# Kernel tuning notes

Hardware: AMD Instinct MI355X
Metric: run time of the kernel (lower is better)

The kernel has to match this reference:

```python
import jax, jax.numpy as jnp
import numpy as np

EPS_LN = 1e-5
EPS_OPM = 1e-3

# dims
S, N, CM, CZ, CH, H, DH = 512, 256, 64, 128, 32, 8, 32
FF = 4 * CM


def _ln(x, w, b):
    mu = jnp.mean(x, axis=-1, keepdims=True)
    var = jnp.mean((x - mu) ** 2, axis=-1, keepdims=True)
    return (x - mu) / jnp.sqrt(var + EPS_LN) * w + b


def setup_inputs() -> dict:
    key = jax.random.key(0)
    ks = jax.random.split(key, 16)
    def w(k, shape):
        return jax.random.normal(k, shape, dtype=jnp.float32) / np.sqrt(shape[0])
    inp = {
        'm': jax.random.normal(ks[0], (S, N, CM), dtype=jnp.float32),
        'z': jax.random.normal(ks[1], (N, N, CZ), dtype=jnp.float32),
        'msa_mask': jnp.ones((S, N), dtype=jnp.float32),
        # OuterProductMean params
        'opm_ln_w': jnp.ones((CM,), jnp.float32), 'opm_ln_b': jnp.zeros((CM,), jnp.float32),
        'opm_w1': w(ks[2], (CM, CH)), 'opm_w2': w(ks[3], (CM, CH)),
        'opm_wout': w(ks[4], (CH * CH, CZ)), 'opm_bout': jnp.zeros((CZ,), jnp.float32),
        # MSAPairWeightedAveraging params
        'pwa_lnm_w': jnp.ones((CM,), jnp.float32), 'pwa_lnm_b': jnp.zeros((CM,), jnp.float32),
        'pwa_lnz_w': jnp.ones((CZ,), jnp.float32), 'pwa_lnz_b': jnp.zeros((CZ,), jnp.float32),
        'pwa_wv': w(ks[5], (CM, H * DH)), 'pwa_wz': w(ks[6], (CZ, H)),
        'pwa_wg': w(ks[7], (CM, H * DH)), 'pwa_wo': w(ks[8], (H * DH, CM)),
        # Transition (SwiGLU, factor 4) params
        'tr_ln_w': jnp.ones((CM,), jnp.float32), 'tr_ln_b': jnp.zeros((CM,), jnp.float32),
        'tr_wa': w(ks[9], (CM, FF)), 'tr_wb': w(ks[10], (CM, FF)), 'tr_wo': w(ks[11], (FF, CM)),
    }
    return inp


def reference(m, z, msa_mask,
              opm_ln_w, opm_ln_b, opm_w1, opm_w2, opm_wout, opm_bout,
              pwa_lnm_w, pwa_lnm_b, pwa_lnz_w, pwa_lnz_b, pwa_wv, pwa_wz, pwa_wg, pwa_wo,
              tr_ln_w, tr_ln_b, tr_wa, tr_wb, tr_wo):
    s, n, cm = m.shape
    h = pwa_wz.shape[1]
    dh = pwa_wv.shape[1] // h
    ch = opm_w1.shape[1]
    # ---- OuterProductMean: z += OPM(m) ----
    mn = _ln(m, opm_ln_w, opm_ln_b)
    mk = msa_mask[..., None]                           # (S, N, 1)
    norm = jnp.einsum('sac,sdc->adc', mk, mk)          # (N, N, 1)
    a = (mn @ opm_w1) * mk                             # (S, N, CH)
    b = (mn @ opm_w2) * mk
    outer = jnp.einsum('sic,sje->ijce', a, b).reshape(n, n, ch * ch)
    z = z + (outer @ opm_wout + opm_bout) / (norm + EPS_OPM)
    # ---- MSAPairWeightedAveraging (residual) ----
    w_att = jax.nn.softmax(_ln(z, pwa_lnz_w, pwa_lnz_b) @ pwa_wz, axis=-2)  # (N, N, H), softmax over j
    mn2 = _ln(m, pwa_lnm_w, pwa_lnm_b)
    v = (mn2 @ pwa_wv).reshape(s, n, h, dh)
    g = jax.nn.sigmoid(mn2 @ pwa_wg).reshape(s, n, h, dh)
    o = jnp.einsum('ijh,sjhd->sihd', w_att, v)
    m = m + (g * o).reshape(s, n, h * dh) @ pwa_wo
    # ---- Transition (SwiGLU, factor 4, residual) ----
    x = _ln(m, tr_ln_w, tr_ln_b)
    m = m + (jax.nn.silu(x @ tr_wa) * (x @ tr_wb)) @ tr_wo
    return (m, z)
```

## Files before the change

### kernel.cpp

```cpp
#include <hip/hip_runtime.h>
#include <hip/hip_bf16.h>

#define S 512
#define N 256
#define CM 64
#define CZ 128
#define CH 32
#define H 8
#define DH 32
#define FF 256
#define HDH 256

typedef __attribute__((ext_vector_type(8))) short bf16x8;
typedef __attribute__((ext_vector_type(4))) float f32x4;

__device__ __forceinline__ float waveReduceSum(float v) {
    #pragma unroll
    for (int off = 32; off > 0; off >>= 1) v += __shfl_xor(v, off);
    return v;
}
__device__ __forceinline__ float waveReduceMax(float v) {
    #pragma unroll
    for (int off = 32; off > 0; off >>= 1) v = fmaxf(v, __shfl_xor(v, off));
    return v;
}
__device__ __forceinline__ unsigned short f2bf(float x) {
    __hip_bfloat16 h = __float2bfloat16(x);
    return *reinterpret_cast<unsigned short*>(&h);
}
__device__ __forceinline__ float bfbits2f(short u) {
    unsigned int x = ((unsigned int)(unsigned short)u) << 16;
    return __uint_as_float(x);
}
__device__ __forceinline__ void gload_lds16(const void* g, void* l) {
    __builtin_amdgcn_global_load_lds(
        (const __attribute__((address_space(1))) unsigned int*)g,
        (__attribute__((address_space(3))) unsigned int*)l, 16, 0, 0);
}

__global__ __launch_bounds__(256) void k0_prep(
    const float* __restrict__ wout, const float* __restrict__ wv,
    const float* __restrict__ wg, const float* __restrict__ wa,
    const float* __restrict__ wb, const float* __restrict__ wo,
    const float* __restrict__ wo2,
    __hip_bfloat16* __restrict__ wout_t, __hip_bfloat16* __restrict__ wv_t,
    __hip_bfloat16* __restrict__ wg_t, __hip_bfloat16* __restrict__ wab_t,
    __hip_bfloat16* __restrict__ wo_t, __hip_bfloat16* __restrict__ wo2_t) {
    int idx = blockIdx.x * 256 + threadIdx.x;
    if (idx < 131072) {
        int f = idx >> 10, k = idx & 1023;
        wout_t[idx] = __float2bfloat16(wout[k * 128 + f]);
    } else if (idx < 147456) {
        int t = idx - 131072; int n = t >> 6, k = t & 63;
        wv_t[t] = __float2bfloat16(wv[k * 256 + n]);
    } else if (idx < 163840) {
        int t = idx - 147456; int n = t >> 6, k = t & 63;
        wg_t[t] = __float2bfloat16(wg[k * 256 + n]);
    } else if (idx < 196608) {
        int t = idx - 163840; int n = t >> 6, k = t & 63;
        wab_t[t] = __float2bfloat16(n < 256 ? wa[k * 256 + n] : wb[k * 256 + (n - 256)]);
    } else if (idx < 212992) {
        int t = idx - 196608; int n = t >> 8, k = t & 255;
        wo_t[t] = __float2bfloat16(wo[k * 64 + n]);
    } else if (idx < 229376) {
        int t = idx - 212992; int n = t >> 8, k = t & 255;
        wo2_t[t] = __float2bfloat16(wo2[k * 64 + n]);
    }
}

__global__ __launch_bounds__(256) void k1_ab(
    const float* __restrict__ m, const float* __restrict__ mask,
    const float* __restrict__ lnw, const float* __restrict__ lnb,
    const float* __restrict__ w1, const float* __restrict__ w2,
    __hip_bfloat16* __restrict__ a_t, __hip_bfloat16* __restrict__ b_t) {
    __shared__ float mn[64][64];
    __shared__ float mk[64];
    int tid = threadIdx.x, w = tid >> 6, lane = tid & 63;
    int i = blockIdx.x >> 3, s0 = (blockIdx.x & 7) * 64;
    float lw = lnw[lane], lb = lnb[lane];
    for (int rr = 0; rr < 16; ++rr) {
        int sl = w * 16 + rr;
        float x = m[((size_t)(s0 + sl) * 256 + i) * 64 + lane];
        float mu = waveReduceSum(x) * (1.0f / 64.0f);
        float d = x - mu;
        float var = waveReduceSum(d * d) * (1.0f / 64.0f);
        mn[sl][lane] = d * rsqrtf(var + 1e-5f) * lw + lb;
        if (lane == 0) mk[sl] = mask[(s0 + sl) * 256 + i];
    }
    __syncthreads();
    int e = lane & 31;
    const float* W = (lane < 32) ? w1 : w2;
    __hip_bfloat16* dst = (lane < 32) ? a_t : b_t;
    float acc[16];
    #pragma unroll
    for (int ss = 0; ss < 16; ++ss) acc[ss] = 0.f;
    for (int c = 0; c < 64; ++c) {
        float wc = W[c * 32 + e];
        #pragma unroll
        for (int ss = 0; ss < 16; ++ss)
            acc[ss] += mn[w * 16 + ss][c] * wc;
    }
    __hip_bfloat16 outv[16];
    #pragma unroll
    for (int ss = 0; ss < 16; ++ss)
        outv[ss] = __float2bfloat16(acc[ss] * mk[w * 16 + ss]);
    __hip_bfloat16* p = dst + (size_t)(i * 32 + e) * 512 + s0 + w * 16;
    *(bf16x8*)p = *(bf16x8*)&outv[0];
    *(bf16x8*)(p + 8) = *(bf16x8*)&outv[8];
}

__global__ __launch_bounds__(256) void k1b_norm(
    const float* __restrict__ mask, float* __restrict__ normb) {
    __shared__ float mcol[512];
    int i = blockIdx.x, t = threadIdx.x;
    mcol[t] = mask[t * 256 + i];
    mcol[t + 256] = mask[(t + 256) * 256 + i];
    __syncthreads();
    float acc = 0.f;
    for (int s = 0; s < 512; ++s) acc += mcol[s] * mask[s * 256 + t];
    normb[i * 256 + t] = acc;
}

__global__ __launch_bounds__(256) void k2_opm(
    const __hip_bfloat16* __restrict__ a_t, const __hip_bfloat16* __restrict__ b_t,
    const __hip_bfloat16* __restrict__ wout_t, const float* __restrict__ bout,
    const float* __restrict__ normb, const float* __restrict__ zin,
    float* __restrict__ zout) {
    __shared__ __align__(16) char smem[32768];
    char* As = smem;
    char* Bs = smem + 8192;
    int tid = threadIdx.x;
    int wid = tid >> 6, lane = tid & 63;
    int g = lane >> 4, lc = lane & 15;
    int bm = blockIdx.x >> 6, bn = blockIdx.x & 63;
    int m0 = bm * 128, n0 = bn * 128;
    int wm = wid >> 1, wn = wid & 1;

    f32x4 acc[4][4];
    #pragma unroll
    for (int fm = 0; fm < 4; ++fm)
        #pragma unroll
        for (int fn = 0; fn < 4; ++fn)
            acc[fm][fn] = (f32x4){0.f, 0.f, 0.f, 0.f};

    for (int k0 = 0; k0 < 512; k0 += 32) {
        __syncthreads();
        #pragma unroll
        for (int h = 0; h < 2; ++h) {
            int c = h * 256 + wid * 64 + lane;
            int r = c >> 2, gs = c & 3;
            int gk = gs ^ ((r >> 1) & 3);
            const __hip_bfloat16* ga = a_t + (size_t)(m0 + r) * 512 + k0 + gk * 8;
            const __hip_bfloat16* gb = b_t + (size_t)(n0 + r) * 512 + k0 + gk * 8;
            gload_lds16(ga, As + h * 4096 + wid * 1024);
            gload_lds16(gb, Bs + h * 4096 + wid * 1024);
        }
        __syncthreads();
        bf16x8 af[4], bfr[4];
        #pragma unroll
        for (int fm = 0; fm < 4; ++fm) {
            int row = wm * 64 + fm * 16 + lc;
            int sw = (g * 16) ^ (((row >> 1) & 3) << 4);
            af[fm] = *(bf16x8*)(As + row * 64 + sw);
        }
        #pragma unroll
        for (int fn = 0; fn < 4; ++fn) {
            int row = wn * 64 + fn * 16 + lc;
            int sw = (g * 16) ^ (((row >> 1) & 3) << 4);
            bfr[fn] = *(bf16x8*)(Bs + row * 64 + sw);
        }
        #pragma unroll
        for (int fm = 0; fm < 4; ++fm)
            #pragma unroll
            for (int fn = 0; fn < 4; ++fn)
                acc[fm][fn] = __builtin_amdgcn_mfma_f32_16x16x32_bf16(
                    af[fm], bfr[fn], acc[fm][fn], 0, 0, 0);
    }
    __syncthreads();
    #pragma unroll
    for (int fm = 0; fm < 4; ++fm) {
        int i_loc = wm * 2 + (fm >> 1);
        #pragma unroll
        for (int fn = 0; fn < 4; ++fn) {
            int j_loc = wn * 2 + (fn >> 1);
            int pair = i_loc * 4 + j_loc;
            int xorp = (pair & 7) << 4;
            #pragma unroll
            for (int r = 0; r < 4; ++r) {
                int mm31 = (fm & 1) * 16 + g * 4 + r;
                int nn31 = (fn & 1) * 16 + lc;
                int off = mm31 * 64 + nn31 * 2;
                int offs = off ^ xorp ^ (((off >> 8) & 3) << 4);
                *(unsigned short*)(smem + pair * 2048 + offs) = f2bf(acc[fm][fn][r]);
            }
        }
    }
    __syncthreads();
    f32x4 acc2[2];
    acc2[0] = (f32x4){0.f, 0.f, 0.f, 0.f};
    acc2[1] = (f32x4){0.f, 0.f, 0.f, 0.f};
    int f0 = wid * 32;
    int pr = lc;
    int xorp2 = (pr & 7) << 4;
    for (int k2 = 0; k2 < 1024; k2 += 32) {
        int offA = k2 * 2 + g * 16;
        int offAs = offA ^ xorp2 ^ (((offA >> 8) & 3) << 4);
        bf16x8 af2 = *(bf16x8*)(smem + pr * 2048 + offAs);
        #pragma unroll
        for (int fn2 = 0; fn2 < 2; ++fn2) {
            int f = f0 + fn2 * 16 + lc;
            bf16x8 bw = *(const bf16x8*)(wout_t + (size_t)f * 1024 + k2 + g * 8);
            acc2[fn2] = __builtin_amdgcn_mfma_f32_16x16x32_bf16(af2, bw, acc2[fn2], 0, 0, 0);
        }
    }
    #pragma unroll
    for (int fn2 = 0; fn2 < 2; ++fn2) {
        #pragma unroll
        for (int r = 0; r < 4; ++r) {
            int pair = g * 4 + r;
            int i = bm * 4 + (pair >> 2), j = bn * 4 + (pair & 3);
            int ij = i * 256 + j;
            int f = f0 + fn2 * 16 + lc;
            float d = acc2[fn2][r];
            zout[(size_t)ij * 128 + f] = zin[(size_t)ij * 128 + f] +
                (d + bout[f]) / (normb[ij] + 1e-3f);
        }
    }
}

__global__ __launch_bounds__(256) void k3_logits(
    const float* __restrict__ zout, const float* __restrict__ lnzw,
    const float* __restrict__ lnzb, const float* __restrict__ wz,
    float* __restrict__ wl) {
    __shared__ float znL[4][128];
    int tid = threadIdx.x, w = tid >> 6, lane = tid & 63;
    int pair = blockIdx.x * 4 + w;
    float z0 = zout[pair * 128 + lane];
    float z1 = zout[pair * 128 + 64 + lane];
    float mu = waveReduceSum(z0 + z1) * (1.0f / 128.0f);
    float d0 = z0 - mu, d1 = z1 - mu;
    float var = waveReduceSum(d0 * d0 + d1 * d1) * (1.0f / 128.0f);
    float rstd = rsqrtf(var + 1e-5f);
    znL[w][lane] = d0 * rstd * lnzw[lane] + lnzb[lane];
    znL[w][lane + 64] = d1 * rstd * lnzw[lane + 64] + lnzb[lane + 64];
    __syncthreads();
    int h = lane >> 3, chunk = lane & 7;
    float p = 0.f;
    #pragma unroll
    for (int cc = 0; cc < 16; ++cc) {
        int c = chunk * 16 + cc;
        p += znL[w][c] * wz[c * 8 + h];
    }
    p += __shfl_xor(p, 1); p += __shfl_xor(p, 2); p += __shfl_xor(p, 4);
    if (chunk == 0) {
        int i = pair >> 8, j = pair & 255;
        wl[(i * 8 + h) * 256 + j] = p;
    }
}

__global__ __launch_bounds__(256) void k4_softmax(
    const float* __restrict__ wl, __hip_bfloat16* __restrict__ wlb) {
    __shared__ float red[8];
    int row = blockIdx.x, t = threadIdx.x;
    int w = t >> 6, lane = t & 63;
    float v = wl[row * 256 + t];
    float mx = waveReduceMax(v);
    if (lane == 0) red[w] = mx;
    __syncthreads();
    mx = fmaxf(fmaxf(red[0], red[1]), fmaxf(red[2], red[3]));
    float ex = expf(v - mx);
    float sm = waveReduceSum(ex);
    if (lane == 0) red[4 + w] = sm;
    __syncthreads();
    float tot = red[4] + red[5] + red[6] + red[7];
    int i = row >> 3, h = row & 7;
    wlb[((h << 8) | i) * 256 + t] = __float2bfloat16(ex / tot);
}

__global__ __launch_bounds__(256) void k5vg(
    const float* __restrict__ m, const float* __restrict__ lnw,
    const float* __restrict__ lnb, const __hip_bfloat16* __restrict__ Bt,
    __hip_bfloat16* __restrict__ out, int mode) {
    __shared__ __align__(16) char As[64 * 128];
    int tid = threadIdx.x, wid = tid >> 6, lane = tid & 63;
    int g = lane >> 4, lc = lane & 15;
    int r0 = blockIdx.x * 64;
    float lw = lnw[lane], lb = lnb[lane];
    for (int rr = 0; rr < 16; ++rr) {
        int lr = wid * 16 + rr;
        float x = m[(size_t)(r0 + lr) * 64 + lane];
        float mu = waveReduceSum(x) * (1.0f / 64.0f);
        float d = x - mu;
        float var = waveReduceSum(d * d) * (1.0f / 64.0f);
        float xn = d * rsqrtf(var + 1e-5f) * lw + lb;
        int byt = lr * 128 + ((lane * 2) ^ ((lr & 7) << 4));
        *(unsigned short*)(As + byt) = f2bf(xn);
    }
    __syncthreads();
    int lr = wid * 16 + lc;
    int swz = (lr & 7) << 4;
    bf16x8 af0 = *(bf16x8*)(As + lr * 128 + ((g * 16) ^ swz));
    bf16x8 af1 = *(bf16x8*)(As + lr * 128 + ((64 + g * 16) ^ swz));
    f32x4 acc[16];
    #pragma unroll
    for (int fn = 0; fn < 16; ++fn) acc[fn] = (f32x4){0.f, 0.f, 0.f, 0.f};
    #pragma unroll
    for (int fn = 0; fn < 16; ++fn) {
        bf16x8 b0 = *(const bf16x8*)&Bt[(fn * 16 + lc) * 64 + g * 8];
        bf16x8 b1 = *(const bf16x8*)&Bt[(fn * 16 + lc) * 64 + 32 + g * 8];
        acc[fn] = __builtin_amdgcn_mfma_f32_16x16x32_bf16(af0, b0, acc[fn], 0, 0, 0);
        acc[fn] = __builtin_amdgcn_mfma_f32_16x16x32_bf16(af1, b1, acc[fn], 0, 0, 0);
    }
    if (mode == 0) {
        #pragma unroll
        for (int fn = 0; fn < 16; ++fn) {
            #pragma unroll
            for (int r = 0; r < 4; ++r) {
                int row = r0 + wid * 16 + g * 4 + r;
                int col = fn * 16 + lc;
                int h = col >> 5, d = col & 31;
                int s = row >> 8, j = row & 255;
                out[(size_t)((h << 14) + (s << 5) + d) * 256 + j] = __float2bfloat16(acc[fn][r]);
            }
        }
    } else {
        #pragma unroll
        for (int fn = 0; fn < 16; ++fn) {
            #pragma unroll
            for (int r = 0; r < 4; ++r) {
                int row = r0 + wid * 16 + g * 4 + r;
                int col = fn * 16 + lc;
                float sg = 1.0f / (1.0f + expf(-acc[fn][r]));
                out[(size_t)row * 256 + col] = __float2bfloat16(sg);
            }
        }
    }
}

__global__ __launch_bounds__(256) void k6a(
    const __hip_bfloat16* __restrict__ vb, const __hip_bfloat16* __restrict__ wlb,
    __hip_bfloat16* __restrict__ obuf) {
    __shared__ __align__(16) char smem[16384];
    char* As = smem;
    char* Bs = smem + 8192;
    int tid = threadIdx.x;
    int wid = tid >> 6, lane = tid & 63;
    int g = lane >> 4, lc = lane & 15;
    int idx = blockIdx.x;
    int h = idx >> 8, rem = idx & 255;
    int bm = rem >> 1, bn = rem & 1;
    int m0 = bm * 128, n0 = bn * 128;
    int wm = wid >> 1, wn = wid & 1;
    const __hip_bfloat16* vb_h = vb + (size_t)h * 16384 * 256;
    const __hip_bfloat16* wlb_h = wlb + (size_t)h * 256 * 256;

    f32x4 acc[4][4];
    #pragma unroll
    for (int fm = 0; fm < 4; ++fm)
        #pragma unroll
        for (int fn = 0; fn < 4; ++fn)
            acc[fm][fn] = (f32x4){0.f, 0.f, 0.f, 0.f};

    for (int k0 = 0; k0 < 256; k0 += 32) {
        __syncthreads();
        #pragma unroll
        for (int hh = 0; hh < 2; ++hh) {
            int c = hh * 256 + wid * 64 + lane;
            int r = c >> 2, gs = c & 3;
            int gk = gs ^ ((r >> 1) & 3);
            const __hip_bfloat16* ga = vb_h + (size_t)(m0 + r) * 256 + k0 + gk * 8;
            const __hip_bfloat16* gb = wlb_h + (size_t)(n0 + r) * 256 + k0 + gk * 8;
            gload_lds16(ga, As + hh * 4096 + wid * 1024);
            gload_lds16(gb, Bs + hh * 4096 + wid * 1024);
        }
        __syncthreads();
        bf16x8 af[4], bfr[4];
        #pragma unroll
        for (int fm = 0; fm < 4; ++fm) {
            int row = wm * 64 + fm * 16 + lc;
            int sw = (g * 16) ^ (((row >> 1) & 3) << 4);
            af[fm] = *(bf16x8*)(As + row * 64 + sw);
        }
        #pragma unroll
        for (int fn = 0; fn < 4; ++fn) {
            int row = wn * 64 + fn * 16 + lc;
            int sw = (g * 16) ^ (((row >> 1) & 3) << 4);
            bfr[fn] = *(bf16x8*)(Bs + row * 64 + sw);
        }
        #pragma unroll
        for (int fm = 0; fm < 4; ++fm)
            #pragma unroll
            for (int fn = 0; fn < 4; ++fn)
                acc[fm][fn] = __builtin_amdgcn_mfma_f32_16x16x32_bf16(
                    af[fm], bfr[fn], acc[fm][fn], 0, 0, 0);
    }
    #pragma unroll
    for (int fm = 0; fm < 4; ++fm) {
        #pragma unroll
        for (int fn = 0; fn < 4; ++fn) {
            #pragma unroll
            for (int r = 0; r < 4; ++r) {
                int mm = m0 + wm * 64 + fm * 16 + g * 4 + r;
                int nn = n0 + wn * 64 + fn * 16 + lc;
                int s = mm >> 5, d = mm & 31;
                obuf[(size_t)(s * 256 + nn) * 256 + h * 32 + d] = __float2bfloat16(acc[fm][fn][r]);
            }
        }
    }
}

__global__ __launch_bounds__(256) void k6b(
    const __hip_bfloat16* __restrict__ obuf, const __hip_bfloat16* __restrict__ gsig,
    const __hip_bfloat16* __restrict__ wo_t, const float* __restrict__ m,
    float* __restrict__ mout) {
    int tid = threadIdx.x, wid = tid >> 6, lane = tid & 63;
    int g = lane >> 4, lc = lane & 15;
    int r0 = blockIdx.x * 128;
    f32x4 acc[2][4];
    #pragma unroll
    for (int fm = 0; fm < 2; ++fm)
        #pragma unroll
        for (int fn = 0; fn < 4; ++fn)
            acc[fm][fn] = (f32x4){0.f, 0.f, 0.f, 0.f};
    for (int ks = 0; ks < 8; ++ks) {
        bf16x8 af[2];
        #pragma unroll
        for (int fm = 0; fm < 2; ++fm) {
            int arow = r0 + wid * 32 + fm * 16 + lc;
            bf16x8 ao = *(const bf16x8*)&obuf[(size_t)arow * 256 + ks * 32 + g * 8];
            bf16x8 ag = *(const bf16x8*)&gsig[(size_t)arow * 256 + ks * 32 + g * 8];
            #pragma unroll
            for (int t = 0; t < 8; ++t)
                af[fm][t] = (short)f2bf(bfbits2f(ao[t]) * bfbits2f(ag[t]));
        }
        #pragma unroll
        for (int fn = 0; fn < 4; ++fn) {
            bf16x8 bf_ = *(const bf16x8*)&wo_t[(fn * 16 + lc) * 256 + ks * 32 + g * 8];
            acc[0][fn] = __builtin_amdgcn_mfma_f32_16x16x32_bf16(af[0], bf_, acc[0][fn], 0, 0, 0);
            acc[1][fn] = __builtin_amdgcn_mfma_f32_16x16x32_bf16(af[1], bf_, acc[1][fn], 0, 0, 0);
        }
    }
    #pragma unroll
    for (int fm = 0; fm < 2; ++fm)
        #pragma unroll
        for (int fn = 0; fn < 4; ++fn)
            #pragma unroll
            for (int r = 0; r < 4; ++r) {
                int row = r0 + wid * 32 + fm * 16 + g * 4 + r;
                int col = fn * 16 + lc;
                mout[(size_t)row * 64 + col] = m[(size_t)row * 64 + col] + acc[fm][fn][r];
            }
}

__global__ __launch_bounds__(256) void k7b(
    const float* __restrict__ mbuf, const float* __restrict__ lnw,
    const float* __restrict__ lnb, const __hip_bfloat16* __restrict__ wab_t,
    __hip_bfloat16* __restrict__ hbuf) {
    __shared__ __align__(16) char As[64 * 128];
    int tid = threadIdx.x, wid = tid >> 6, lane = tid & 63;
    int g = lane >> 4, lc = lane & 15;
    int r0 = blockIdx.x * 64;
    float lw = lnw[lane], lb = lnb[lane];
    for (int rr = 0; rr < 16; ++rr) {
        int lr = wid * 16 + rr;
        float x = mbuf[(size_t)(r0 + lr) * 64 + lane];
        float mu = waveReduceSum(x) * (1.0f / 64.0f);
        float d = x - mu;
        float var = waveReduceSum(d * d) * (1.0f / 64.0f);
        float xn = d * rsqrtf(var + 1e-5f) * lw + lb;
        int byt = lr * 128 + ((lane * 2) ^ ((lr & 7) << 4));
        *(unsigned short*)(As + byt) = f2bf(xn);
    }
    __syncthreads();
    int lr = wid * 16 + lc;
    int swz = (lr & 7) << 4;
    bf16x8 af0 = *(bf16x8*)(As + lr * 128 + ((g * 16) ^ swz));
    bf16x8 af1 = *(bf16x8*)(As + lr * 128 + ((64 + g * 16) ^ swz));
    f32x4 acc[32];
    #pragma unroll
    for (int fn = 0; fn < 32; ++fn) acc[fn] = (f32x4){0.f, 0.f, 0.f, 0.f};
    #pragma unroll
    for (int fn = 0; fn < 32; ++fn) {
        bf16x8 b0 = *(const bf16x8*)&wab_t[(fn * 16 + lc) * 64 + g * 8];
        bf16x8 b1 = *(const bf16x8*)&wab_t[(fn * 16 + lc) * 64 + 32 + g * 8];
        acc[fn] = __builtin_amdgcn_mfma_f32_16x16x32_bf16(af0, b0, acc[fn], 0, 0, 0);
        acc[fn] = __builtin_amdgcn_mfma_f32_16x16x32_bf16(af1, b1, acc[fn], 0, 0, 0);
    }
    #pragma unroll
    for (int fn = 0; fn < 16; ++fn) {
        #pragma unroll
        for (int r = 0; r < 4; ++r) {
            int row = r0 + wid * 16 + g * 4 + r;
            int f = fn * 16 + lc;
            float aa = acc[fn][r];
            float bb = acc[fn + 16][r];
            float sil = aa / (1.0f + expf(-aa));
            hbuf[(size_t)row * 256 + f] = __float2bfloat16(sil * bb);
        }
    }
}

__global__ __launch_bounds__(256) void k7c(
    const __hip_bfloat16* __restrict__ hbuf, const __hip_bfloat16* __restrict__ wo2_t,
    float* __restrict__ mout) {
    int tid = threadIdx.x, wid = tid >> 6, lane = tid & 63;
    int g = lane >> 4, lc = lane & 15;
    int r0 = blockIdx.x * 128;
    f32x4 acc[2][4];
    #pragma unroll
    for (int fm = 0; fm < 2; ++fm)
        #pragma unroll
        for (int fn = 0; fn < 4; ++fn)
            acc[fm][fn] = (f32x4){0.f, 0.f, 0.f, 0.f};
    for (int ks = 0; ks < 8; ++ks) {
        bf16x8 af[2];
        #pragma unroll
        for (int fm = 0; fm < 2; ++fm) {
            int arow = r0 + wid * 32 + fm * 16 + lc;
            af[fm] = *(const bf16x8*)&hbuf[(size_t)arow * 256 + ks * 32 + g * 8];
        }
        #pragma unroll
        for (int fn = 0; fn < 4; ++fn) {
            bf16x8 bf_ = *(const bf16x8*)&wo2_t[(fn * 16 + lc) * 256 + ks * 32 + g * 8];
            acc[0][fn] = __builtin_amdgcn_mfma_f32_16x16x32_bf16(af[0], bf_, acc[0][fn], 0, 0, 0);
            acc[1][fn] = __builtin_amdgcn_mfma_f32_16x16x32_bf16(af[1], bf_, acc[1][fn], 0, 0, 0);
        }
    }
    #pragma unroll
    for (int fm = 0; fm < 2; ++fm)
        #pragma unroll
        for (int fn = 0; fn < 4; ++fn)
            #pragma unroll
            for (int r = 0; r < 4; ++r) {
                int row = r0 + wid * 32 + fm * 16 + g * 4 + r;
                int col = fn * 16 + lc;
                mout[(size_t)row * 64 + col] += acc[fm][fn][r];
            }
}

extern "C" void kernel_launch(void* const* d_in, const int* in_sizes, int n_in,
                              void* d_out, int out_size, void* d_ws, size_t ws_size,
                              hipStream_t stream) {
    const float* m        = (const float*)d_in[0];
    const float* z        = (const float*)d_in[1];
    const float* mask     = (const float*)d_in[2];
    const float* opm_ln_w = (const float*)d_in[3];
    const float* opm_ln_b = (const float*)d_in[4];
    const float* opm_w1   = (const float*)d_in[5];
    const float* opm_w2   = (const float*)d_in[6];
    const float* opm_wout = (const float*)d_in[7];
    const float* opm_bout = (const float*)d_in[8];
    const float* pwa_lnm_w = (const float*)d_in[9];
    const float* pwa_lnm_b = (const float*)d_in[10];
    const float* pwa_lnz_w = (const float*)d_in[11];
    const float* pwa_lnz_b = (const float*)d_in[12];
    const float* pwa_wv   = (const float*)d_in[13];
    const float* pwa_wz   = (const float*)d_in[14];
    const float* pwa_wg   = (const float*)d_in[15];
    const float* pwa_wo   = (const float*)d_in[16];
    const float* tr_ln_w  = (const float*)d_in[17];
    const float* tr_ln_b  = (const float*)d_in[18];
    const float* tr_wa    = (const float*)d_in[19];
    const float* tr_wb    = (const float*)d_in[20];
    const float* tr_wo    = (const float*)d_in[21];

    float* m_out = (float*)d_out;
    float* z_out = m_out + (size_t)S * N * CM;

    char* w = (char*)d_ws;
    __hip_bfloat16* wout_t = (__hip_bfloat16*)w;
    __hip_bfloat16* wv_t   = (__hip_bfloat16*)(w + 262144);
    __hip_bfloat16* wg_t   = (__hip_bfloat16*)(w + 294912);
    __hip_bfloat16* wab_t  = (__hip_bfloat16*)(w + 327680);
    __hip_bfloat16* wo_t   = (__hip_bfloat16*)(w + 393216);
    __hip_bfloat16* wo2_t  = (__hip_bfloat16*)(w + 425984);
    float* normb           = (float*)(w + 458752);
    float* wl              = (float*)(w + 720896);
    __hip_bfloat16* wlb    = (__hip_bfloat16*)(w + 2818048);
    char* bufA             = w + 3866624;
    char* bufB             = w + 70975488;

    __hip_bfloat16* a_t  = (__hip_bfloat16*)bufA;
    __hip_bfloat16* b_t  = a_t + 4194304;
    __hip_bfloat16* vb   = (__hip_bfloat16*)bufA;
    __hip_bfloat16* gsig = (__hip_bfloat16*)bufA;
    __hip_bfloat16* obuf = (__hip_bfloat16*)bufB;
    __hip_bfloat16* hbuf = (__hip_bfloat16*)bufB;

    k0_prep<<<896, 256, 0, stream>>>(opm_wout, pwa_wv, pwa_wg, tr_wa, tr_wb, pwa_wo, tr_wo,
                                     wout_t, wv_t, wg_t, wab_t, wo_t, wo2_t);
    k1_ab<<<2048, 256, 0, stream>>>(m, mask, opm_ln_w, opm_ln_b, opm_w1, opm_w2, a_t, b_t);
    k1b_norm<<<N, 256, 0, stream>>>(mask, normb);
    k2_opm<<<4096, 256, 0, stream>>>(a_t, b_t, wout_t, opm_bout, normb, z, z_out);
    k3_logits<<<N * N / 4, 256, 0, stream>>>(z_out, pwa_lnz_w, pwa_lnz_b, pwa_wz, wl);
    k4_softmax<<<N * H, 256, 0, stream>>>(wl, wlb);
    k5vg<<<2048, 256, 0, stream>>>(m, pwa_lnm_w, pwa_lnm_b, wv_t, vb, 0);
    k6a<<<2048, 256, 0, stream>>>(vb, wlb, obuf);
    k5vg<<<2048, 256, 0, stream>>>(m, pwa_lnm_w, pwa_lnm_b, wg_t, gsig, 1);
    k6b<<<1024, 256, 0, stream>>>(obuf, gsig, wo_t, m, m_out);
    k7b<<<2048, 256, 0, stream>>>(m_out, tr_ln_w, tr_ln_b, wab_t, hbuf);
    k7c<<<1024, 256, 0, stream>>>(hbuf, wo2_t, m_out);
}
```

Baseline: 827.0 us.

## Double-buffer LDS in OPM and attention GEMMs; fuse gate, output projection and transition kernel

Adds two-stage LDS double buffering to the k2_opm and k6a GEMM main loops, so the next K tile's global-to-LDS loads are issued before computing on the current tile and one barrier per iteration is removed. It also fuses the sigmoid gate computation, gated output projection plus residual, transition LayerNorm, SwiGLU and output projection into a single per-64-row kernel. The gate and hidden activations stay in shared memory instead of round-tripping through global bf16 buffers, and four launches collapse to one. In exchange, shared memory per block grows (about 58KB in the fused kernel, 32KB in the GEMMs), which may lower occupancy.

```diff
diff --git a/kernel.cpp b/kernel.cpp
--- a/kernel.cpp
+++ b/kernel.cpp
@@ -127,8 +127,6 @@
     const float* __restrict__ normb, const float* __restrict__ zin,
     float* __restrict__ zout) {
     __shared__ __align__(16) char smem[32768];
-    char* As = smem;
-    char* Bs = smem + 8192;
     int tid = threadIdx.x;
     int wid = tid >> 6, lane = tid & 63;
     int g = lane >> 4, lc = lane & 15;
@@ -136,6 +134,7 @@
     int m0 = bm * 128, n0 = bn * 128;
     int wm = wid >> 1, wn = wid & 1;
 
+    int c_ = wid * 64 + lane;
     f32x4 acc[4][4];
     #pragma unroll
     for (int fm = 0; fm < 4; ++fm)
@@ -143,19 +142,26 @@
         for (int fn = 0; fn < 4; ++fn)
             acc[fm][fn] = (f32x4){0.f, 0.f, 0.f, 0.f};
 
-    for (int k0 = 0; k0 < 512; k0 += 32) {
-        __syncthreads();
+    auto stage = [&](int sel, int k0) {
         #pragma unroll
         for (int h = 0; h < 2; ++h) {
-            int c = h * 256 + wid * 64 + lane;
+            int c = h * 256 + c_;
             int r = c >> 2, gs = c & 3;
             int gk = gs ^ ((r >> 1) & 3);
             const __hip_bfloat16* ga = a_t + (size_t)(m0 + r) * 512 + k0 + gk * 8;
             const __hip_bfloat16* gb = b_t + (size_t)(n0 + r) * 512 + k0 + gk * 8;
-            gload_lds16(ga, As + h * 4096 + wid * 1024);
-            gload_lds16(gb, Bs + h * 4096 + wid * 1024);
-        }
-        __syncthreads();
+            gload_lds16(ga, smem + sel * 16384 + h * 4096 + wid * 1024);
+            gload_lds16(gb, smem + sel * 16384 + 8192 + h * 4096 + wid * 1024);
+        }
+    };
+
+    stage(0, 0);
+    __syncthreads();
+    int cur = 0;
+    for (int t = 0; t < 16; ++t) {
+        if (t < 15) stage(cur ^ 1, (t + 1) * 32);
+        char* As = smem + cur * 16384;
+        char* Bs = As + 8192;
         bf16x8 af[4], bfr[4];
         #pragma unroll
         for (int fm = 0; fm < 4; ++fm) {
@@ -175,8 +181,9 @@
             for (int fn = 0; fn < 4; ++fn)
                 acc[fm][fn] = __builtin_amdgcn_mfma_f32_16x16x32_bf16(
                     af[fm], bfr[fn], acc[fm][fn], 0, 0, 0);
-    }
-    __syncthreads();
+        __syncthreads();
+        cur ^= 1;
+    }
     #pragma unroll
     for (int fm = 0; fm < 4; ++fm) {
         int i_loc = wm * 2 + (fm >> 1);
@@ -277,10 +284,10 @@
     wlb[((h << 8) | i) * 256 + t] = __float2bfloat16(ex / tot);
 }
 
-__global__ __launch_bounds__(256) void k5vg(
+__global__ __launch_bounds__(256) void k5v(
     const float* __restrict__ m, const float* __restrict__ lnw,
     const float* __restrict__ lnb, const __hip_bfloat16* __restrict__ Bt,
-    __hip_bfloat16* __restrict__ out, int mode) {
+    __hip_bfloat16* __restrict__ out) {
     __shared__ __align__(16) char As[64 * 128];
     int tid = threadIdx.x, wid = tid >> 6, lane = tid & 63;
     int g = lane >> 4, lc = lane & 15;
@@ -311,28 +318,15 @@
         acc[fn] = __builtin_amdgcn_mfma_f32_16x16x32_bf16(af0, b0, acc[fn], 0, 0, 0);
         acc[fn] = __builtin_amdgcn_mfma_f32_16x16x32_bf16(af1, b1, acc[fn], 0, 0, 0);
     }
-    if (mode == 0) {
-        #pragma unroll
-        for (int fn = 0; fn < 16; ++fn) {
-            #pragma unroll
-            for (int r = 0; r < 4; ++r) {
-                int row = r0 + wid * 16 + g * 4 + r;
-                int col = fn * 16 + lc;
-                int h = col >> 5, d = col & 31;
-                int s = row >> 8, j = row & 255;
-                out[(size_t)((h << 14) + (s << 5) + d) * 256 + j] = __float2bfloat16(acc[fn][r]);
-            }
-        }
-    } else {
-        #pragma unroll
-        for (int fn = 0; fn < 16; ++fn) {
-            #pragma unroll
-            for (int r = 0; r < 4; ++r) {
-                int row = r0 + wid * 16 + g * 4 + r;
-                int col = fn * 16 + lc;
-                float sg = 1.0f / (1.0f + expf(-acc[fn][r]));
-                out[(size_t)row * 256 + col] = __float2bfloat16(sg);
-            }
+    #pragma unroll
+    for (int fn = 0; fn < 16; ++fn) {
+        #pragma unroll
+        for (int r = 0; r < 4; ++r) {
+            int row = r0 + wid * 16 + g * 4 + r;
+            int col = fn * 16 + lc;
+            int h = col >> 5, d = col & 31;
+            int s = row >> 8, j = row & 255;
+            out[(size_t)((h << 14) + (s << 5) + d) * 256 + j] = __float2bfloat16(acc[fn][r]);
         }
     }
 }
@@ -340,9 +334,7 @@
 __global__ __launch_bounds__(256) void k6a(
     const __hip_bfloat16* __restrict__ vb, const __hip_bfloat16* __restrict__ wlb,
     __hip_bfloat16* __restrict__ obuf) {
-    __shared__ __align__(16) char smem[16384];
-    char* As = smem;
-    char* Bs = smem + 8192;
+    __shared__ __align__(16) char smem[32768];
     int tid = threadIdx.x;
     int wid = tid >> 6, lane = tid & 63;
     int g = lane >> 4, lc = lane & 15;
@@ -353,6 +345,7 @@
     int wm = wid >> 1, wn = wid & 1;
     const __hip_bfloat16* vb_h = vb + (size_t)h * 16384 * 256;
     const __hip_bfloat16* wlb_h = wlb + (size_t)h * 256 * 256;
+    int c_ = wid * 64 + lane;
 
     f32x4 acc[4][4];
     #pragma unroll
@@ -361,19 +354,26 @@
         for (int fn = 0; fn < 4; ++fn)
             acc[fm][fn] = (f32x4){0.f, 0.f, 0.f, 0.f};
 
-    for (int k0 = 0; k0 < 256; k0 += 32) {
-        __syncthreads();
+    auto stage = [&](int sel, int k0) {
         #pragma unroll
         for (int hh = 0; hh < 2; ++hh) {
-            int c = hh * 256 + wid * 64 + lane;
+            int c = hh * 256 + c_;
             int r = c >> 2, gs = c & 3;
             int gk = gs ^ ((r >> 1) & 3);
             const __hip_bfloat16* ga = vb_h + (size_t)(m0 + r) * 256 + k0 + gk * 8;
             const __hip_bfloat16* gb = wlb_h + (size_t)(n0 + r) * 256 + k0 + gk * 8;
-            gload_lds16(ga, As + hh * 4096 + wid * 1024);
-            gload_lds16(gb, Bs + hh * 4096 + wid * 1024);
-        }
-        __syncthreads();
+            gload_lds16(ga, smem + sel * 16384 + hh * 4096 + wid * 1024);
+            gload_lds16(gb, smem + sel * 16384 + 8192 + hh * 4096 + wid * 1024);
+        }
+    };
+
+    stage(0, 0);
+    __syncthreads();
+    int cur = 0;
+    for (int t = 0; t < 8; ++t) {
+        if (t < 7) stage(cur ^ 1, (t + 1) * 32);
+        char* As = smem + cur * 16384;
+        char* Bs = As + 8192;
         bf16x8 af[4], bfr[4];
         #pragma unroll
         for (int fm = 0; fm < 4; ++fm) {
@@ -393,6 +393,8 @@
             for (int fn = 0; fn < 4; ++fn)
                 acc[fm][fn] = __builtin_amdgcn_mfma_f32_16x16x32_bf16(
                     af[fm], bfr[fn], acc[fm][fn], 0, 0, 0);
+        __syncthreads();
+        cur ^= 1;
     }
     #pragma unroll
     for (int fm = 0; fm < 4; ++fm) {
@@ -409,133 +411,140 @@
     }
 }
 
-__global__ __launch_bounds__(256) void k6b(
-    const __hip_bfloat16* __restrict__ obuf, const __hip_bfloat16* __restrict__ gsig,
-    const __hip_bfloat16* __restrict__ wo_t, const float* __restrict__ m,
+__global__ __launch_bounds__(256) void k67(
+    const float* __restrict__ m,
+    const float* __restrict__ lnmw, const float* __restrict__ lnmb,
+    const __hip_bfloat16* __restrict__ wg_t, const __hip_bfloat16* __restrict__ wo_t,
+    const __hip_bfloat16* __restrict__ obuf,
+    const float* __restrict__ trlnw, const float* __restrict__ trlnb,
+    const __hip_bfloat16* __restrict__ wab_t, const __hip_bfloat16* __restrict__ wo2_t,
     float* __restrict__ mout) {
-    int tid = threadIdx.x, wid = tid >> 6, lane = tid & 63;
-    int g = lane >> 4, lc = lane & 15;
-    int r0 = blockIdx.x * 128;
-    f32x4 acc[2][4];
-    #pragma unroll
-    for (int fm = 0; fm < 2; ++fm)
-        #pragma unroll
-        for (int fn = 0; fn < 4; ++fn)
-            acc[fm][fn] = (f32x4){0.f, 0.f, 0.f, 0.f};
-    for (int ks = 0; ks < 8; ++ks) {
-        bf16x8 af[2];
-        #pragma unroll
-        for (int fm = 0; fm < 2; ++fm) {
-            int arow = r0 + wid * 32 + fm * 16 + lc;
-            bf16x8 ao = *(const bf16x8*)&obuf[(size_t)arow * 256 + ks * 32 + g * 8];
-            bf16x8 ag = *(const bf16x8*)&gsig[(size_t)arow * 256 + ks * 32 + g * 8];
-            #pragma unroll
-            for (int t = 0; t < 8; ++t)
-                af[fm][t] = (short)f2bf(bfbits2f(ao[t]) * bfbits2f(ag[t]));
-        }
-        #pragma unroll
-        for (int fn = 0; fn < 4; ++fn) {
-            bf16x8 bf_ = *(const bf16x8*)&wo_t[(fn * 16 + lc) * 256 + ks * 32 + g * 8];
-            acc[0][fn] = __builtin_amdgcn_mfma_f32_16x16x32_bf16(af[0], bf_, acc[0][fn], 0, 0, 0);
-            acc[1][fn] = __builtin_amdgcn_mfma_f32_16x16x32_bf16(af[1], bf_, acc[1][fn], 0, 0, 0);
-        }
-    }
-    #pragma unroll
-    for (int fm = 0; fm < 2; ++fm)
-        #pragma unroll
-        for (int fn = 0; fn < 4; ++fn)
-            #pragma unroll
-            for (int r = 0; r < 4; ++r) {
-                int row = r0 + wid * 32 + fm * 16 + g * 4 + r;
-                int col = fn * 16 + lc;
-                mout[(size_t)row * 64 + col] = m[(size_t)row * 64 + col] + acc[fm][fn][r];
-            }
-}
-
-__global__ __launch_bounds__(256) void k7b(
-    const float* __restrict__ mbuf, const float* __restrict__ lnw,
-    const float* __restrict__ lnb, const __hip_bfloat16* __restrict__ wab_t,
-    __hip_bfloat16* __restrict__ hbuf) {
-    __shared__ __align__(16) char As[64 * 128];
+    __shared__ __align__(16) char xnS[8192];
+    __shared__ __align__(16) char ghS[32768];
+    __shared__ float mnS[64][68];
     int tid = threadIdx.x, wid = tid >> 6, lane = tid & 63;
     int g = lane >> 4, lc = lane & 15;
     int r0 = blockIdx.x * 64;
-    float lw = lnw[lane], lb = lnb[lane];
-    for (int rr = 0; rr < 16; ++rr) {
-        int lr = wid * 16 + rr;
-        float x = mbuf[(size_t)(r0 + lr) * 64 + lane];
-        float mu = waveReduceSum(x) * (1.0f / 64.0f);
-        float d = x - mu;
-        float var = waveReduceSum(d * d) * (1.0f / 64.0f);
-        float xn = d * rsqrtf(var + 1e-5f) * lw + lb;
-        int byt = lr * 128 + ((lane * 2) ^ ((lr & 7) << 4));
-        *(unsigned short*)(As + byt) = f2bf(xn);
-    }
-    __syncthreads();
     int lr = wid * 16 + lc;
     int swz = (lr & 7) << 4;
-    bf16x8 af0 = *(bf16x8*)(As + lr * 128 + ((g * 16) ^ swz));
-    bf16x8 af1 = *(bf16x8*)(As + lr * 128 + ((64 + g * 16) ^ swz));
-    f32x4 acc[32];
-    #pragma unroll
-    for (int fn = 0; fn < 32; ++fn) acc[fn] = (f32x4){0.f, 0.f, 0.f, 0.f};
-    #pragma unroll
-    for (int fn = 0; fn < 32; ++fn) {
-        bf16x8 b0 = *(const bf16x8*)&wab_t[(fn * 16 + lc) * 64 + g * 8];
-        bf16x8 b1 = *(const bf16x8*)&wab_t[(fn * 16 + lc) * 64 + 32 + g * 8];
-        acc[fn] = __builtin_amdgcn_mfma_f32_16x16x32_bf16(af0, b0, acc[fn], 0, 0, 0);
-        acc[fn] = __builtin_amdgcn_mfma_f32_16x16x32_bf16(af1, b1, acc[fn], 0, 0, 0);
-    }
-    #pragma unroll
-    for (int fn = 0; fn < 16; ++fn) {
-        #pragma unroll
-        for (int r = 0; r < 4; ++r) {
-            int row = r0 + wid * 16 + g * 4 + r;
-            int f = fn * 16 + lc;
-            float aa = acc[fn][r];
-            float bb = acc[fn + 16][r];
-            float sil = aa / (1.0f + expf(-aa));
-            hbuf[(size_t)row * 256 + f] = __float2bfloat16(sil * bb);
-        }
-    }
-}
-
-__global__ __launch_bounds__(256) void k7c(
-    const __hip_bfloat16* __restrict__ hbuf, const __hip_bfloat16* __restrict__ wo2_t,
-    float* __restrict__ mout) {
-    int tid = threadIdx.x, wid = tid >> 6, lane = tid & 63;
-    int g = lane >> 4, lc = lane & 15;
-    int r0 = blockIdx.x * 128;
-    f32x4 acc[2][4];
-    #pragma unroll
-    for (int fm = 0; fm < 2; ++fm)
+
+    {
+        float lw = lnmw[lane], lb = lnmb[lane];
+        for (int rr = 0; rr < 16; ++rr) {
+            int r2 = wid * 16 + rr;
+            float x = m[(size_t)(r0 + r2) * 64 + lane];
+            float mu = waveReduceSum(x) * (1.0f / 64.0f);
+            float d = x - mu;
+            float var = waveReduceSum(d * d) * (1.0f / 64.0f);
+            float xn = d * rsqrtf(var + 1e-5f) * lw + lb;
+            *(unsigned short*)(xnS + r2 * 128 + ((lane * 2) ^ ((r2 & 7) << 4))) = f2bf(xn);
+        }
+    }
+    __syncthreads();
+    {
+        bf16x8 af0 = *(bf16x8*)(xnS + lr * 128 + ((g * 16) ^ swz));
+        bf16x8 af1 = *(bf16x8*)(xnS + lr * 128 + ((64 + g * 16) ^ swz));
+        #pragma unroll
+        for (int fn = 0; fn < 16; ++fn) {
+            f32x4 a_ = (f32x4){0.f, 0.f, 0.f, 0.f};
+            bf16x8 b0 = *(const bf16x8*)&wg_t[(fn * 16 + lc) * 64 + g * 8];
+            bf16x8 b1 = *(const bf16x8*)&wg_t[(fn * 16 + lc) * 64 + 32 + g * 8];
+            a_ = __builtin_amdgcn_mfma_f32_16x16x32_bf16(af0, b0, a_, 0, 0, 0);
+            a_ = __builtin_amdgcn_mfma_f32_16x16x32_bf16(af1, b1, a_, 0, 0, 0);
+            #pragma unroll
+            for (int r = 0; r < 4; ++r) {
+                int row = wid * 16 + g * 4 + r, col = fn * 16 + lc;
+                float sg = 1.0f / (1.0f + expf(-a_[r]));
+                *(unsigned short*)(ghS + row * 512 + ((col * 2) ^ ((row & 7) << 4))) = f2bf(sg);
+            }
+        }
+    }
+    __syncthreads();
+    {
+        f32x4 acc[4];
+        #pragma unroll
+        for (int fn = 0; fn < 4; ++fn) acc[fn] = (f32x4){0.f, 0.f, 0.f, 0.f};
+        for (int ks = 0; ks < 8; ++ks) {
+            bf16x8 ao = *(const bf16x8*)&obuf[(size_t)(r0 + lr) * 256 + ks * 32 + g * 8];
+            bf16x8 ag = *(bf16x8*)(ghS + lr * 512 + ((ks * 64 + g * 16) ^ swz));
+            bf16x8 af;
+            #pragma unroll
+            for (int t = 0; t < 8; ++t)
+                af[t] = (short)f2bf(bfbits2f(ao[t]) * bfbits2f(ag[t]));
+            #pragma unroll
+            for (int fn = 0; fn < 4; ++fn) {
+                bf16x8 bf_ = *(const bf16x8*)&wo_t[(fn * 16 + lc) * 256 + ks * 32 + g * 8];
+                acc[fn] = __builtin_amdgcn_mfma_f32_16x16x32_bf16(af, bf_, acc[fn], 0, 0, 0);
+            }
+        }
         #pragma unroll
         for (int fn = 0; fn < 4; ++fn)
-            acc[fm][fn] = (f32x4){0.f, 0.f, 0.f, 0.f};
-    for (int ks = 0; ks < 8; ++ks) {
-        bf16x8 af[2];
-        #pragma unroll
-        for (int fm = 0; fm < 2; ++fm) {
-            int arow = r0 + wid * 32 + fm * 16 + lc;
-            af[fm] = *(const bf16x8*)&hbuf[(size_t)arow * 256 + ks * 32 + g * 8];
-        }
-        #pragma unroll
-        for (int fn = 0; fn < 4; ++fn) {
-            bf16x8 bf_ = *(const bf16x8*)&wo2_t[(fn * 16 + lc) * 256 + ks * 32 + g * 8];
-            acc[0][fn] = __builtin_amdgcn_mfma_f32_16x16x32_bf16(af[0], bf_, acc[0][fn], 0, 0, 0);
-            acc[1][fn] = __builtin_amdgcn_mfma_f32_16x16x32_bf16(af[1], bf_, acc[1][fn], 0, 0, 0);
-        }
-    }
-    #pragma unroll
-    for (int fm = 0; fm < 2; ++fm)
+            #pragma unroll
+            for (int r = 0; r < 4; ++r) {
+                int row = wid * 16 + g * 4 + r, col = fn * 16 + lc;
+                mnS[row][col] = m[(size_t)(r0 + row) * 64 + col] + acc[fn][r];
+            }
+    }
+    __syncthreads();
+    {
+        float lw = trlnw[lane], lb = trlnb[lane];
+        for (int rr = 0; rr < 16; ++rr) {
+            int r2 = wid * 16 + rr;
+            float x = mnS[r2][lane];
+            float mu = waveReduceSum(x) * (1.0f / 64.0f);
+            float d = x - mu;
+            float var = waveReduceSum(d * d) * (1.0f / 64.0f);
+            float xn = d * rsqrtf(var + 1e-5f) * lw + lb;
+            *(unsigned short*)(xnS + r2 * 128 + ((lane * 2) ^ ((r2 & 7) << 4))) = f2bf(xn);
+        }
+    }
+    __syncthreads();
+    {
+        bf16x8 af0 = *(bf16x8*)(xnS + lr * 128 + ((g * 16) ^ swz));
+        bf16x8 af1 = *(bf16x8*)(xnS + lr * 128 + ((64 + g * 16) ^ swz));
+        f32x4 acc[32];
+        #pragma unroll
+        for (int fn = 0; fn < 32; ++fn) acc[fn] = (f32x4){0.f, 0.f, 0.f, 0.f};
+        #pragma unroll
+        for (int fn = 0; fn < 32; ++fn) {
+            bf16x8 b0 = *(const bf16x8*)&wab_t[(fn * 16 + lc) * 64 + g * 8];
+            bf16x8 b1 = *(const bf16x8*)&wab_t[(fn * 16 + lc) * 64 + 32 + g * 8];
+            acc[fn] = __builtin_amdgcn_mfma_f32_16x16x32_bf16(af0, b0, acc[fn], 0, 0, 0);
+            acc[fn] = __builtin_amdgcn_mfma_f32_16x16x32_bf16(af1, b1, acc[fn], 0, 0, 0);
+        }
+        #pragma unroll
+        for (int fn = 0; fn < 16; ++fn) {
+            #pragma unroll
+            for (int r = 0; r < 4; ++r) {
+                int row = wid * 16 + g * 4 + r, f = fn * 16 + lc;
+                float aa = acc[fn][r];
+                float bb = acc[fn + 16][r];
+                float sil = aa / (1.0f + expf(-aa));
+                *(unsigned short*)(ghS + row * 512 + ((f * 2) ^ ((row & 7) << 4))) = f2bf(sil * bb);
+            }
+        }
+    }
+    __syncthreads();
+    {
+        f32x4 acc[4];
+        #pragma unroll
+        for (int fn = 0; fn < 4; ++fn) acc[fn] = (f32x4){0.f, 0.f, 0.f, 0.f};
+        for (int ks = 0; ks < 8; ++ks) {
+            bf16x8 af = *(bf16x8*)(ghS + lr * 512 + ((ks * 64 + g * 16) ^ swz));
+            #pragma unroll
+            for (int fn = 0; fn < 4; ++fn) {
+                bf16x8 bf_ = *(const bf16x8*)&wo2_t[(fn * 16 + lc) * 256 + ks * 32 + g * 8];
+                acc[fn] = __builtin_amdgcn_mfma_f32_16x16x32_bf16(af, bf_, acc[fn], 0, 0, 0);
+            }
+        }
         #pragma unroll
         for (int fn = 0; fn < 4; ++fn)
             #pragma unroll
             for (int r = 0; r < 4; ++r) {
-                int row = r0 + wid * 32 + fm * 16 + g * 4 + r;
-                int col = fn * 16 + lc;
-                mout[(size_t)row * 64 + col] += acc[fm][fn][r];
-            }
+                int row = wid * 16 + g * 4 + r, col = fn * 16 + lc;
+                mout[(size_t)(r0 + row) * 64 + col] = mnS[row][col] + acc[fn][r];
+            }
+    }
 }
 
 extern "C" void kernel_launch(void* const* d_in, const int* in_sizes, int n_in,
@@ -583,9 +592,7 @@
     __hip_bfloat16* a_t  = (__hip_bfloat16*)bufA;
     __hip_bfloat16* b_t  = a_t + 4194304;
     __hip_bfloat16* vb   = (__hip_bfloat16*)bufA;
-    __hip_bfloat16* gsig = (__hip_bfloat16*)bufA;
     __hip_bfloat16* obuf = (__hip_bfloat16*)bufB;
-    __hip_bfloat16* hbuf = (__hip_bfloat16*)bufB;
 
     k0_prep<<<896, 256, 0, stream>>>(opm_wout, pwa_wv, pwa_wg, tr_wa, tr_wb, pwa_wo, tr_wo,
                                      wout_t, wv_t, wg_t, wab_t, wo_t, wo2_t);
@@ -594,10 +601,8 @@
     k2_opm<<<4096, 256, 0, stream>>>(a_t, b_t, wout_t, opm_bout, normb, z, z_out);
     k3_logits<<<N * N / 4, 256, 0, stream>>>(z_out, pwa_lnz_w, pwa_lnz_b, pwa_wz, wl);
     k4_softmax<<<N * H, 256, 0, stream>>>(wl, wlb);
-    k5vg<<<2048, 256, 0, stream>>>(m, pwa_lnm_w, pwa_lnm_b, wv_t, vb, 0);
+    k5v<<<2048, 256, 0, stream>>>(m, pwa_lnm_w, pwa_lnm_b, wv_t, vb);
     k6a<<<2048, 256, 0, stream>>>(vb, wlb, obuf);
-    k5vg<<<2048, 256, 0, stream>>>(m, pwa_lnm_w, pwa_lnm_b, wg_t, gsig, 1);
-    k6b<<<1024, 256, 0, stream>>>(obuf, gsig, wo_t, m, m_out);
-    k7b<<<2048, 256, 0, stream>>>(m_out, tr_ln_w, tr_ln_b, wab_t, hbuf);
-    k7c<<<1024, 256, 0, stream>>>(hbuf, wo2_t, m_out);
-}
+    k67<<<2048, 256, 0, stream>>>(m, pwa_lnm_w, pwa_lnm_b, wg_t, wo_t, obuf,
+                                  tr_ln_w, tr_ln_b, wab_t, wo2_t, m_out);
+}
```

New measurement: 804.7 us. -2.7%, faster.
